# Performance work log

Hardware: AMD Instinct MI355X
Metric: run time of the kernel (lower is better)

## Reference

```python
import jax, jax.numpy as jnp
import numpy as np

# dims
B, L, HID = 4, 4096, 1024
H, D = 16, 64            # num_mem_heads, head_dim = HID // H
DM = 128                 # mem_intermediate = head_dim * mem_expansion_factor (2.0)
K = 4                    # conv_kernel
CS = 64                  # chunk_size
EPS = 1e-6


def setup_inputs() -> dict:
    key = jax.random.key(0)
    ks = jax.random.split(key, 16)
    std = 0.02
    f = lambda i, shape: jax.random.normal(ks[i], shape, jnp.float32) * std
    return {
        'hidden_states': jax.random.normal(ks[0], (B, L, HID), jnp.float32),
        'Wq': f(1, (HID, HID)), 'Wk': f(2, (HID, HID)), 'Wv': f(3, (HID, HID)),
        'conv_q_w': f(4, (HID, K)), 'conv_q_b': jnp.zeros((HID,), jnp.float32),
        'conv_k_w': f(5, (HID, K)), 'conv_k_b': jnp.zeros((HID,), jnp.float32),
        'conv_v_w': f(6, (HID, K)), 'conv_v_b': jnp.zeros((HID,), jnp.float32),
        'q_norm_w': jnp.ones((D,), jnp.float32), 'k_norm_w': jnp.ones((D,), jnp.float32),
        'mem_decay_w': f(7, (H, HID)), 'mem_decay_b': jnp.zeros((H,), jnp.float32),
        'surprise_w': f(8, (H, HID)), 'surprise_b': jnp.zeros((H,), jnp.float32),
        'lr_w': f(9, (H, HID)), 'lr_b': jnp.zeros((H,), jnp.float32),
        'W1': f(10, (H, D, DM)), 'W2': f(11, (H, DM, D)),
    }


def _silu_bwd(x):
    sig = jax.nn.sigmoid(x)
    return sig + jax.nn.silu(x) * (1.0 - sig)


def _rmsnorm(x, w):
    xf = x.astype(jnp.float32)
    var = jnp.mean(xf * xf, axis=-1, keepdims=True)
    return w * (xf * jax.lax.rsqrt(var + EPS)).astype(x.dtype)


def _causal_conv_silu(x, w, b):
    # x: [B, L, H, D] -> depthwise causal conv over time on C=H*D channels -> [B, H, L, D]
    Bs, Ls, Hh, Dd = x.shape
    xc = jnp.swapaxes(x.reshape(Bs, Ls, Hh * Dd), 1, 2)        # [B, C, L]
    xp = jnp.pad(xc, ((0, 0), (0, 0), (K - 1, 0)))             # left pad -> causal
    y = b[None, :, None]
    for k in range(K):
        y = y + w[None, :, k:k + 1] * xp[:, :, k:k + Ls]
    y = jax.nn.silu(y)
    return jnp.swapaxes(y.reshape(Bs, Hh, Dd, Ls), -2, -1)     # [B, H, L, D]


def _decayed_scan(d, v, init):
    # y_t = d_t * y_{t-1} + v_t, y_0 = init; d: [B,H,C,1], v: [B,H,C,dim], init: [B,H,1,dim]
    def comb(x, y):
        a1, b1 = x
        a2, b2 = y
        return a1 * a2, b1 * a2 + b2
    A, Bv = jax.lax.associative_scan(comb, (d, v), axis=2)
    return A * init + Bv


def _forward(hidden_states, Wq, Wk, Wv, conv_q_w, conv_q_b, conv_k_w, conv_k_b,
             conv_v_w, conv_v_b, q_norm_w, k_norm_w, mem_decay_w, mem_decay_b,
             surprise_w, surprise_b, lr_w, lr_b, W1, W2):
    x = hidden_states
    # projections -> [B, L, H, D]
    q = (x @ Wq.T).reshape(B, L, H, D)
    k = (x @ Wk.T).reshape(B, L, H, D)
    v = (x @ Wv.T).reshape(B, L, H, D)
    # depthwise causal conv + silu -> [B, H, L, D]
    q = _causal_conv_silu(q, conv_q_w, conv_q_b)
    k = _causal_conv_silu(k, conv_k_w, conv_k_b)
    v = _causal_conv_silu(v, conv_v_w, conv_v_b)
    # QK RMSNorm (per head_dim)
    q = _rmsnorm(q, q_norm_w)
    k = _rmsnorm(k, k_norm_w)
    # per-timestep gates -> [B, H, L, 1]
    mem_decay = 1.0 - jax.nn.sigmoid(x @ mem_decay_w.T + mem_decay_b)
    surprise_decay = jax.nn.sigmoid(x @ surprise_w.T + surprise_b)
    lr = jax.nn.sigmoid(x @ lr_w.T + lr_b)
    to_gate = lambda g: jnp.swapaxes(g, -2, -1)[..., None]
    mem_decay, surprise_decay, lr = to_gate(mem_decay), to_gate(surprise_decay), to_gate(lr)

    # split sequence into chunks: [N, B, H, CS, *]
    N = L // CS
    ch = lambda t: jnp.moveaxis(t.reshape(B, H, N, CS, t.shape[-1]), 2, 0)
    qs, ks_, vs = ch(q), ch(k), ch(v)
    mds, sds, lrs = ch(mem_decay), ch(surprise_decay), ch(lr)

    W1b = jnp.broadcast_to(W1[None], (B, H, D, DM))
    W2b = jnp.broadcast_to(W2[None], (B, H, DM, D))
    carry0 = (W1b, W2b,
              jnp.zeros((B, H, 1, DM), jnp.float32),   # W1_surprise
              jnp.zeros((B, H, 1, D), jnp.float32),    # W2_surprise
              jnp.zeros((B, H, 1, D), jnp.float32),    # key_momentum
              jnp.zeros((B, H, 1, DM), jnp.float32))   # X1_momentum

    def step(carry, inp):
        W1c, W2c, W1s, W2s, kmom, xmom = carry
        qc, kc, vc, md, sd, lrc = inp
        # memory MLP fwd with chunk-frozen weights
        Z1 = kc @ W1c                       # [B,H,CS,DM]
        X1 = jax.nn.silu(Z1)
        mems = X1 @ W2c                     # [B,H,CS,D]
        g_m = mems - vc
        g_Z1 = (g_m @ jnp.swapaxes(W2c, -2, -1)) * _silu_bwd(Z1)
        g_m = -lrc * g_m
        g_Z1 = -lrc * g_Z1
        # activation-space surprise/momentum scans (decayed linear recurrence)
        W1s_n = _decayed_scan(sd, g_Z1, W1s)[:, :, -1:, :]
        W2s_n = _decayed_scan(sd, g_m, W2s)[:, :, -1:, :]
        kmom_n = _decayed_scan(md, kc, kmom)[:, :, -1:, :]
        xmom_n = _decayed_scan(md, X1, xmom)[:, :, -1:, :]
        # weight update at chunk boundary: decay + outer-product of accumulated factors
        mprod = jnp.prod(md, axis=2, keepdims=True)          # [B,H,1,1]
        W1n = mprod * W1c + jnp.swapaxes(kmom_n, -2, -1) @ W1s_n
        W2n = mprod * W2c + jnp.swapaxes(xmom_n, -2, -1) @ W2s_n
        # retrieve with updated memory
        y = jax.nn.silu(qc @ W1n) @ W2n                      # [B,H,CS,D]
        return (W1n, W2n, W1s_n, W2s_n, kmom_n, xmom_n), y

    _, ys = jax.lax.scan(step, carry0, (qs, ks_, vs, mds, sds, lrs))
    mem_states = jnp.moveaxis(ys, 0, 2).reshape(B, H, L, D)
    # replicate torch: mem_states.transpose(-2,-1).reshape(B, L, H*D)
    return jnp.swapaxes(mem_states, -2, -1).reshape(B, L, H * D)


def reference(hidden_states, Wq, Wk, Wv, conv_q_w, conv_q_b, conv_k_w, conv_k_b,
              conv_v_w, conv_v_b, q_norm_w, k_norm_w, mem_decay_w, mem_decay_b,
              surprise_w, surprise_b, lr_w, lr_b, W1, W2):
    return _forward(hidden_states, Wq, Wk, Wv, conv_q_w, conv_q_b, conv_k_w, conv_k_b,
                    conv_v_w, conv_v_b, q_norm_w, k_norm_w, mem_decay_w, mem_decay_b,
                    surprise_w, surprise_b, lr_w, lr_b, W1, W2)
```

## Files before the change

kernel.cpp:

```cpp
#include <hip/hip_runtime.h>

#define B_ 4
#define L_ 4096
#define HID_ 1024
#define H_ 16
#define D_ 64
#define DM_ 128
#define CS_ 64
#define NCH_ 64
#define EPS_ 1e-6f

typedef __attribute__((ext_vector_type(8))) short bfrag_t;
typedef __attribute__((ext_vector_type(4))) float facc_t;

#define MFMA16(a,b,c) __builtin_amdgcn_mfma_f32_16x16x32_bf16(a,b,c,0,0,0)

__device__ __forceinline__ float sigf(float x){ return 1.0f/(1.0f + __expf(-x)); }

__device__ __forceinline__ unsigned f2bfu(float x){
  unsigned u = __float_as_uint(x);
  return (u + 0x7fffu + ((u>>16)&1u)) >> 16;
}
__device__ __forceinline__ float bf2f(unsigned short s){
  return __uint_as_float(((unsigned)s)<<16);
}

#define DPP_ADD_(x, ctrl) x += __int_as_float(__builtin_amdgcn_update_dpp(0, __float_as_int(x), ctrl, 0xf, 0xf, true))
__device__ __forceinline__ float wsum64(float x){
  DPP_ADD_(x, 0x111);
  DPP_ADD_(x, 0x112);
  DPP_ADD_(x, 0x114);
  DPP_ADD_(x, 0x118);
  const float a = __int_as_float(__builtin_amdgcn_readlane(__float_as_int(x), 15));
  const float b = __int_as_float(__builtin_amdgcn_readlane(__float_as_int(x), 31));
  const float c = __int_as_float(__builtin_amdgcn_readlane(__float_as_int(x), 47));
  const float d = __int_as_float(__builtin_amdgcn_readlane(__float_as_int(x), 63));
  return (a+b)+(c+d);
}

__global__ __launch_bounds__(256) void cast_kernel(
    const float* __restrict__ x,  const float* __restrict__ wq,
    const float* __restrict__ wk, const float* __restrict__ wv,
    unsigned short* __restrict__ xb,  unsigned short* __restrict__ wqb,
    unsigned short* __restrict__ wkb, unsigned short* __restrict__ wvb)
{
  const int bid = blockIdx.x;
  const float* s; unsigned short* d; int base;
  if (bid < 16384){ s = x; d = xb; base = bid*1024; }
  else {
    int r = bid - 16384; const int a = r >> 10; r &= 1023; base = r*1024;
    s = (a==0)?wq:(a==1)?wk:wv;
    d = (a==0)?wqb:(a==1)?wkb:wvb;
  }
  const int i = base + threadIdx.x*4;
  float4 v = *(const float4*)(s + i);
  unsigned lo = f2bfu(v.x) | (f2bfu(v.y)<<16);
  unsigned hi = f2bfu(v.z) | (f2bfu(v.w)<<16);
  uint2 o; o.x = lo; o.y = hi;
  *(uint2*)(d + i) = o;
}

__global__ __launch_bounds__(256, 2) void gemm_bf16_nt(
    const unsigned short* __restrict__ A, const unsigned short* __restrict__ Bw,
    unsigned short* __restrict__ C, int M, int N, int K)
{
  __shared__ __align__(16) unsigned short As[128*32];
  __shared__ __align__(16) unsigned short Bs[128*32];
  const int tid = threadIdx.x;
  const int lane = tid & 63, wave = tid >> 6;
  const int lq = lane & 15, quad = lane >> 4;
  const int m0 = blockIdx.y*128, n0 = blockIdx.x*128;
  const int row = tid >> 2, ks = (tid & 3)*8;
  const int mo = (wave & 1)*64, no = (wave >> 1)*64;

  const unsigned short* pa0 = A  + (size_t)(m0 + row)*K + ks;
  const unsigned short* pa1 = pa0 + (size_t)64*K;
  const unsigned short* pb0 = Bw + (size_t)(n0 + row)*K + ks;
  const unsigned short* pb1 = pb0 + (size_t)64*K;

  uint4 ra0 = *(const uint4*)pa0;
  uint4 ra1 = *(const uint4*)pa1;
  uint4 rb0 = *(const uint4*)pb0;
  uint4 rb1 = *(const uint4*)pb1;

  facc_t acc[4][4];
  #pragma unroll
  for (int i=0;i<4;++i)
    #pragma unroll
    for (int j=0;j<4;++j) acc[i][j] = (facc_t){0.f,0.f,0.f,0.f};

  const int kiters = K >> 5;
  for (int kt = 0; kt < kiters; ++kt){
    *(uint4*)&As[row*32 + ks]      = ra0;
    *(uint4*)&As[(row+64)*32 + ks] = ra1;
    *(uint4*)&Bs[row*32 + ks]      = rb0;
    *(uint4*)&Bs[(row+64)*32 + ks] = rb1;
    __syncthreads();
    if (kt+1 < kiters){
      const int off = (kt+1)*32;
      ra0 = *(const uint4*)(pa0 + off);
      ra1 = *(const uint4*)(pa1 + off);
      rb0 = *(const uint4*)(pb0 + off);
      rb1 = *(const uint4*)(pb1 + off);
    }
    bfrag_t af[4], bf[4];
    #pragma unroll
    for (int mt=0;mt<4;++mt) af[mt] = *(const bfrag_t*)&As[(mo+mt*16+lq)*32 + quad*8];
    #pragma unroll
    for (int nt=0;nt<4;++nt) bf[nt] = *(const bfrag_t*)&Bs[(no+nt*16+lq)*32 + quad*8];
    #pragma unroll
    for (int mt=0;mt<4;++mt)
      #pragma unroll
      for (int nt=0;nt<4;++nt)
        acc[mt][nt] = MFMA16(af[mt], bf[nt], acc[mt][nt]);
    __syncthreads();
  }

  #pragma unroll
  for (int mt=0;mt<4;++mt)
    #pragma unroll
    for (int nt=0;nt<4;++nt)
      #pragma unroll
      for (int r=0;r<4;++r){
        const int rr = m0 + mo + mt*16 + quad*4 + r;
        const int cc = n0 + no + nt*16 + lq;
        const int t = cc >> 10, hh = (cc >> 6) & 15, dd = cc & 63;
        const int b = rr >> 12, l = rr & 4095;
        C[((((size_t)t*B_ + b)*H_ + hh)*L_ + l)*64 + dd]
            = (unsigned short)f2bfu(acc[mt][nt][r]);
      }
}

__global__ __launch_bounds__(256, 2) void gates_kernel(
  const float* __restrict__ x,
  const float* __restrict__ mdw, const float* __restrict__ mdb,
  const float* __restrict__ sw,  const float* __restrict__ sb,
  const float* __restrict__ lw,  const float* __restrict__ lb,
  float* __restrict__ cmb, float* __restrict__ c1b, float* __restrict__ ppb)
{
  __shared__ float xs[64][68];
  __shared__ float wg[48][68];
  const int tid = threadIdx.x;
  const int m0 = blockIdx.x * 64;
  const int tx = tid & 15, ty = tid >> 4;
  float acc[4][3];
  #pragma unroll
  for (int r=0;r<4;++r){ acc[r][0]=0.f; acc[r][1]=0.f; acc[r][2]=0.f; }

  for (int k0 = 0; k0 < HID_; k0 += 64){
    {
      const int r = tid >> 2, kq = tid & 3;
      const float* xp = x + (size_t)(m0 + r) * HID_ + k0 + kq*16;
      #pragma unroll
      for (int u=0;u<4;++u){
        float4 v = *(const float4*)(xp + u*4);
        *(float4*)&xs[r][kq*16 + u*4] = v;
      }
    }
    #pragma unroll
    for (int u=0;u<3;++u){
      const int idx = tid + 256*u;
      const int gi = idx >> 4, q = idx & 15;
      const float* wp = (gi < 16) ? (mdw + (size_t)gi*HID_)
                      : (gi < 32) ? (sw  + (size_t)(gi-16)*HID_)
                                  : (lw  + (size_t)(gi-32)*HID_);
      float4 v = *(const float4*)(wp + k0 + q*4);
      *(float4*)&wg[gi][q*4] = v;
    }
    __syncthreads();
    for (int kk=0; kk<64; ++kk){
      float xv[4], wv[3];
      #pragma unroll
      for (int r=0;r<4;++r) xv[r] = xs[ty*4+r][kk];
      #pragma unroll
      for (int gg=0;gg<3;++gg) wv[gg] = wg[tx*3+gg][kk];
      #pragma unroll
      for (int r=0;r<4;++r)
        #pragma unroll
        for (int gg=0;gg<3;++gg) acc[r][gg] += xv[r]*wv[gg];
    }
    __syncthreads();
  }

  float (*ls)[68] = xs;
  #pragma unroll
  for (int gg=0; gg<3; ++gg){
    const int gi = tx*3 + gg;
    const int s = gi >> 4, hh = gi & 15;
    const float bias = (s==0) ? mdb[hh] : (s==1) ? sb[hh] : lb[hh];
    #pragma unroll
    for (int r=0;r<4;++r) ls[gi][ty*4+r] = acc[r][gg] + bias;
  }
  __syncthreads();

  const int lane = tid & 63, wv2 = tid >> 6;
  const int b = m0 >> 12, n = (m0 & 4095) >> 6;
  #pragma unroll
  for (int u=0;u<4;++u){
    const int hh = wv2*4 + u;
    const float md = 1.0f - sigf(ls[hh][lane]);
    const float sd = sigf(ls[16+hh][lane]);
    const float lr = sigf(ls[32+hh][lane]);
    float vm = md, vs = sd;
    #pragma unroll
    for (int off = 1; off < 64; off <<= 1){
      float om = __shfl_down(vm, off);
      float os = __shfl_down(vs, off);
      if (lane + off < 64){ vm *= om; vs *= os; }
    }
    float mex = __shfl_down(vm, 1);
    float sex = __shfl_down(vs, 1);
    if (lane == 63){ mex = 1.0f; sex = 1.0f; }
    const size_t base = ((size_t)(b*16 + hh)*NCH_ + n)*64;
    cmb[base + lane] = mex;
    c1b[base + lane] = -lr * sex;
    if (lane == 0){
      ppb[((size_t)(b*16+hh)*NCH_ + n)*2 + 0] = vm;
      ppb[((size_t)(b*16+hh)*NCH_ + n)*2 + 1] = vs;
    }
  }
}

#define HALO_T_ ((size_t)64*64*3*64)

__global__ __launch_bounds__(192) void halo_kernel(
  const unsigned short* __restrict__ qg, const unsigned short* __restrict__ kg,
  const unsigned short* __restrict__ vg, unsigned short* __restrict__ halo)
{
  const int blk = blockIdx.x;
  const int bh = blk / 63;
  const int ch = blk % 63 + 1;
  const int tid = threadIdx.x;
  const int tt = tid >> 6, lane = tid & 63;
  const long src = ((long)bh*L_ + (long)ch*64 - 3 + tt)*64 + lane;
  const long dst = (((long)bh*64 + ch)*3 + tt)*64 + lane;
  halo[dst]               = qg[src];
  halo[dst +   HALO_T_]   = kg[src];
  halo[dst + 2*HALO_T_]   = vg[src];
}

__global__ __launch_bounds__(256) void prep_kernel(
  unsigned short* __restrict__ qg, unsigned short* __restrict__ kg,
  unsigned short* __restrict__ vg,
  const unsigned short* __restrict__ halo,
  const float* __restrict__ cmg,
  const float* __restrict__ cqw, const float* __restrict__ cqb,
  const float* __restrict__ ckw, const float* __restrict__ ckb,
  const float* __restrict__ cvw, const float* __restrict__ cvb,
  const float* __restrict__ qnw, const float* __restrict__ knw,
  float* __restrict__ kredg)
{
  const int blk = blockIdx.x;
  const int bh = blk >> 6, ch = blk & 63;
  const int tid = threadIdx.x;
  const int lane = tid & 63, wave = tid >> 6;
  const int h = bh & 15;
  const int c = h*64 + lane;

  float wq4[4], wk4[4], wv4[4];
  #pragma unroll
  for (int kk=0;kk<4;++kk){ wq4[kk]=cqw[c*4+kk]; wk4[kk]=ckw[c*4+kk]; wv4[kk]=cvw[c*4+kk]; }
  const float bq = cqb[c], bk = ckb[c], bv = cvb[c];
  const float qnf = qnw[lane], knf = knw[lane];

  const long base = ((long)bh*L_ + (long)ch*64)*64 + lane;
  const int r0 = wave*16;

  float qw_[3], kw_[3], vw_[3];
  #pragma unroll
  for (int t=0;t<3;++t){
    const int row = r0 - 3 + t;
    if (row >= 0){
      qw_[t] = bf2f(qg[base + (long)row*64]);
      kw_[t] = bf2f(kg[base + (long)row*64]);
      vw_[t] = bf2f(vg[base + (long)row*64]);
    } else if (ch == 0){
      qw_[t] = 0.f; kw_[t] = 0.f; vw_[t] = 0.f;
    } else {
      const long hb = (((long)bh*64 + ch)*3 + (row + 3))*64 + lane;
      qw_[t] = bf2f(halo[hb]);
      kw_[t] = bf2f(halo[hb +   HALO_T_]);
      vw_[t] = bf2f(halo[hb + 2*HALO_T_]);
    }
  }
  __syncthreads();

  const float* cmp = cmg + ((size_t)bh*NCH_ + ch)*64;
  float kp = 0.f;
  #pragma unroll 8
  for (int i=0;i<16;++i){
    const int row = r0 + i;
    const long a = base + (long)row*64;
    const float q0v = bf2f(qg[a]);
    const float k0v = bf2f(kg[a]);
    const float v0v = bf2f(vg[a]);
    float aq = bq + wq4[0]*qw_[0] + wq4[1]*qw_[1] + wq4[2]*qw_[2] + wq4[3]*q0v;
    float ak = bk + wk4[0]*kw_[0] + wk4[1]*kw_[1] + wk4[2]*kw_[2] + wk4[3]*k0v;
    float av = bv + wv4[0]*vw_[0] + wv4[1]*vw_[1] + wv4[2]*vw_[2] + wv4[3]*v0v;
    const float yk = ak*sigf(ak), yq = aq*sigf(aq), yv = av*sigf(av);
    const float ssk = wsum64(yk*yk);
    const float ssq = wsum64(yq*yq);
    const float vk = knf * yk * rsqrtf(ssk*(1.0f/64.0f) + EPS_);
    const float vq = qnf * yq * rsqrtf(ssq*(1.0f/64.0f) + EPS_);
    const unsigned short kb16 = (unsigned short)f2bfu(vk);
    qg[a] = (unsigned short)f2bfu(vq);
    kg[a] = kb16;
    vg[a] = (unsigned short)f2bfu(yv);
    kp += cmp[row] * bf2f(kb16);
    qw_[0]=qw_[1]; qw_[1]=qw_[2]; qw_[2]=q0v;
    kw_[0]=kw_[1]; kw_[1]=kw_[2]; kw_[2]=k0v;
    vw_[0]=vw_[1]; vw_[1]=vw_[2]; vw_[2]=v0v;
  }

  __shared__ float kpart[4][64];
  kpart[wave][lane] = kp;
  __syncthreads();
  if (wave == 0)
    kredg[((size_t)bh*NCH_ + ch)*64 + lane] =
        (kpart[0][lane]+kpart[1][lane]) + (kpart[2][lane]+kpart[3][lane]);
}

#define SK 72
#define SX 136

__global__ __launch_bounds__(1024, 4) void scan_kernel(
  const unsigned short* __restrict__ qg, const unsigned short* __restrict__ kg,
  const unsigned short* __restrict__ vg,
  const float* __restrict__ cmg, const float* __restrict__ c1g,
  const float* __restrict__ ppg, const float* __restrict__ krg,
  const float* __restrict__ W1in, const float* __restrict__ W2in,
  float* __restrict__ out)
{
  const int bh = blockIdx.x;
  const int h = bh & 15;
  const int tid = threadIdx.x;
  const int lane = tid & 63, wave = tid >> 6;
  const int lq = lane & 15, quad = lane >> 4;
  const int rw = (wave & 3) * 16;
  const int cw = wave >> 2;

  __shared__ __align__(16) unsigned short sm[63488];
  unsigned short* xbs = sm + 27648;
  unsigned short* W1T = sm + 36352;
  unsigned short* W2n = sm + 45568;
  unsigned short* W2T = sm + 54784;
  __shared__ float cmA[2][64], c1A[2][64], krA[2][64], ppS[2][2];
  __shared__ float kmomS[64], xmomS[128], w1momS[128], w2momS[64];

  {
    const int j = tid >> 3, q0 = (tid & 7) * 8;
    const float* w1p = W1in + (size_t)h * D_ * DM_;
    #pragma unroll
    for (int t=0;t<8;++t)
      W1T[j*SK + q0 + t] = (unsigned short)f2bfu(w1p[(size_t)(q0+t)*DM_ + j]);
    const float* w2p = W2in + (size_t)h * DM_ * D_ + (size_t)j*D_ + q0;
    #pragma unroll
    for (int t=0;t<8;++t){
      unsigned short v = (unsigned short)f2bfu(w2p[t]);
      W2n[j*SK + q0 + t] = v;
      W2T[(q0+t)*SX + j] = v;
    }
  }
  if (tid < 64){ kmomS[tid]=0.f; w2momS[tid]=0.f; }
  if (tid < 128){ xmomS[tid]=0.f; w1momS[tid]=0.f; }

  const long cbase = (long)bh * L_ * 64;
  const int tr = tid >> 4, tc = (tid & 15) * 4;

  uint2 rq2, rk2, rv2;
  float cmr=0.f, c1r=0.f, krr=0.f, ppr=0.f;

  auto stage_load = [&](int m){
    if (m >= NCH_) return;
    const long a = cbase + ((long)m*64 + tr)*64 + tc;
    rq2 = *(const uint2*)(qg + a);
    rk2 = *(const uint2*)(kg + a);
    rv2 = *(const uint2*)(vg + a);
    if (wave == 0){
      cmr = cmg[((size_t)bh*NCH_ + m)*64 + lane];
      c1r = c1g[((size_t)bh*NCH_ + m)*64 + lane];
      krr = krg[((size_t)bh*NCH_ + m)*64 + lane];
    }
    if (tid < 2) ppr = ppg[((size_t)bh*NCH_ + m)*2 + tid];
  };

  auto stage_store = [&](int m, int s){
    if (m >= NCH_) return;
    unsigned short* kc = sm + s*4608;
    unsigned short* qc = sm + 9216 + s*4608;
    unsigned short* gm = sm + 18432 + s*4608;
    *(uint2*)&kc[tr*SK + tc] = rk2;
    *(uint2*)&qc[tr*SK + tc] = rq2;
    *(uint2*)&gm[tr*SK + tc] = rv2;
    if (wave == 0){ cmA[s][lane] = cmr; c1A[s][lane] = c1r; krA[s][lane] = krr; }
    if (tid < 2) ppS[s][tid] = ppr;
  };

  stage_load(0);
  stage_store(0, 0);
  __syncthreads();

  for (int n = 0; n < NCH_; ++n){
    const int cur = n & 1, nxt = cur ^ 1;
    const unsigned short* kcs = sm + cur*4608;
    const unsigned short* qcs = sm + 9216 + cur*4608;
    unsigned short* gms = sm + 18432 + cur*4608;

    stage_load(n+1);

    facc_t zk[2];
    {
      const bfrag_t a0 = *(const bfrag_t*)&kcs[(rw+lq)*SK + quad*8];
      const bfrag_t a1 = *(const bfrag_t*)&kcs[(rw+lq)*SK + 32 + quad*8];
      #pragma unroll
      for (int nt=0;nt<2;++nt){
        const int j = cw*32 + nt*16 + lq;
        const bfrag_t b0 = *(const bfrag_t*)&W1T[j*SK + quad*8];
        const bfrag_t b1 = *(const bfrag_t*)&W1T[j*SK + 32 + quad*8];
        facc_t z = {0.f,0.f,0.f,0.f};
        z = MFMA16(a0,b0,z); z = MFMA16(a1,b1,z);
        zk[nt] = z;
        const int r0 = rw + quad*4;
        #pragma unroll
        for (int r=0;r<4;++r)
          xbs[(r0+r)*SX + j] = (unsigned short)f2bfu(z[r]*sigf(z[r]));
      }
    }
    __syncthreads();

    {
      bfrag_t xa[4];
      #pragma unroll
      for (int kt=0;kt<4;++kt) xa[kt] = *(const bfrag_t*)&xbs[(rw+lq)*SX + kt*32 + quad*8];
      const int e = cw*16 + lq;
      facc_t z = {0.f,0.f,0.f,0.f};
      #pragma unroll
      for (int kt=0;kt<4;++kt){
        const bfrag_t bb = *(const bfrag_t*)&W2T[e*SX + kt*32 + quad*8];
        z = MFMA16(xa[kt], bb, z);
      }
      const int r0 = rw + quad*4;
      #pragma unroll
      for (int r=0;r<4;++r){
        const float g = z[r] - bf2f(gms[(r0+r)*SK + e]);
        gms[(r0+r)*SK + e] = (unsigned short)f2bfu(g);
      }
    }
    if (tid < 64) kmomS[tid] = ppS[cur][0]*kmomS[tid] + krA[cur][tid];
    {
      const int j = tid >> 3, s8 = tid & 7;
      float a0 = 0.f, a1 = 0.f;
      #pragma unroll
      for (int ii=0; ii<8; ii+=2){
        const int i0 = s8*8 + ((ii     + s8) & 7);
        const int i1 = s8*8 + ((ii + 1 + s8) & 7);
        a0 += cmA[cur][i0] * bf2f(xbs[i0*SX + j]);
        a1 += cmA[cur][i1] * bf2f(xbs[i1*SX + j]);
      }
      float xp = a0 + a1;
      xp += __shfl_xor(xp, 1);
      xp += __shfl_xor(xp, 2);
      xp += __shfl_xor(xp, 4);
      if (s8 == 0) xmomS[j] = ppS[cur][0]*xmomS[j] + xp;
    }
    stage_store(n+1, nxt);
    __syncthreads();

    {
      const bfrag_t a0 = *(const bfrag_t*)&gms[(rw+lq)*SK + quad*8];
      const bfrag_t a1 = *(const bfrag_t*)&gms[(rw+lq)*SK + 32 + quad*8];
      #pragma unroll
      for (int nt=0;nt<2;++nt){
        const int j = cw*32 + nt*16 + lq;
        const bfrag_t b0 = *(const bfrag_t*)&W2n[j*SK + quad*8];
        const bfrag_t b1 = *(const bfrag_t*)&W2n[j*SK + 32 + quad*8];
        facc_t gz = {0.f,0.f,0.f,0.f};
        gz = MFMA16(a0,b0,gz); gz = MFMA16(a1,b1,gz);
        const int r0 = rw + quad*4;
        #pragma unroll
        for (int r=0;r<4;++r){
          const float zz = zk[nt][r];
          const float sg = sigf(zz);
          xbs[(r0+r)*SX + j] = (unsigned short)f2bfu(gz[r] * (sg * (1.0f + zz*(1.0f - sg))));
        }
      }
    }
    __syncthreads();

    {
      const int j = tid >> 3, s8 = tid & 7;
      float a0 = 0.f, a1 = 0.f;
      #pragma unroll
      for (int ii=0; ii<8; ii+=2){
        const int i0 = s8*8 + ((ii     + s8) & 7);
        const int i1 = s8*8 + ((ii + 1 + s8) & 7);
        a0 += c1A[cur][i0] * bf2f(xbs[i0*SX + j]);
        a1 += c1A[cur][i1] * bf2f(xbs[i1*SX + j]);
      }
      float wp = a0 + a1;
      wp += __shfl_xor(wp, 1);
      wp += __shfl_xor(wp, 2);
      wp += __shfl_xor(wp, 4);
      if (s8 == 0) w1momS[j] = ppS[cur][1]*w1momS[j] + wp;
    }
    {
      const int e = tid >> 4, s16 = tid & 15;
      float a0 = 0.f, a1 = 0.f;
      #pragma unroll
      for (int ii=0; ii<4; ii+=2){
        const int i0 = s16*4 + ((ii     + s16) & 3);
        const int i1 = s16*4 + ((ii + 1 + s16) & 3);
        a0 += c1A[cur][i0] * bf2f(gms[i0*SK + e]);
        a1 += c1A[cur][i1] * bf2f(gms[i1*SK + e]);
      }
      float wp = a0 + a1;
      wp += __shfl_xor(wp, 1);
      wp += __shfl_xor(wp, 2);
      wp += __shfl_xor(wp, 4);
      wp += __shfl_xor(wp, 8);
      if (s16 == 0) w2momS[e] = ppS[cur][1]*w2momS[e] + wp;
    }
    __syncthreads();

    {
      const float Pmd = ppS[cur][0];
      const int j = tid >> 3, q0 = (tid & 7)*8;
      const float wm = w1momS[j], xm = xmomS[j];
      {
        const int off = j*SK + q0;
        bfrag_t wv = *(const bfrag_t*)&W1T[off];
        alignas(16) unsigned short o[8];
        #pragma unroll
        for (int s2=0;s2<8;++s2)
          o[s2] = (unsigned short)f2bfu(Pmd*bf2f((unsigned short)wv[s2]) + wm*kmomS[q0+s2]);
        *(bfrag_t*)&W1T[off] = *(const bfrag_t*)o;
      }
      {
        const int off = j*SK + q0;
        bfrag_t wv = *(const bfrag_t*)&W2n[off];
        alignas(16) unsigned short o[8];
        #pragma unroll
        for (int s2=0;s2<8;++s2)
          o[s2] = (unsigned short)f2bfu(Pmd*bf2f((unsigned short)wv[s2]) + xm*w2momS[q0+s2]);
        *(bfrag_t*)&W2n[off] = *(const bfrag_t*)o;
      }
      const int e2 = tid >> 4, js = (tid & 15)*8;
      const float w2m = w2momS[e2];
      {
        const int off = e2*SX + js;
        bfrag_t wv = *(const bfrag_t*)&W2T[off];
        alignas(16) unsigned short o[8];
        #pragma unroll
        for (int s2=0;s2<8;++s2)
          o[s2] = (unsigned short)f2bfu(Pmd*bf2f((unsigned short)wv[s2]) + xmomS[js+s2]*w2m);
        *(bfrag_t*)&W2T[off] = *(const bfrag_t*)o;
      }
    }
    __syncthreads();

    {
      const bfrag_t a0 = *(const bfrag_t*)&qcs[(rw+lq)*SK + quad*8];
      const bfrag_t a1 = *(const bfrag_t*)&qcs[(rw+lq)*SK + 32 + quad*8];
      #pragma unroll
      for (int nt=0;nt<2;++nt){
        const int j = cw*32 + nt*16 + lq;
        const bfrag_t b0 = *(const bfrag_t*)&W1T[j*SK + quad*8];
        const bfrag_t b1 = *(const bfrag_t*)&W1T[j*SK + 32 + quad*8];
        facc_t z = {0.f,0.f,0.f,0.f};
        z = MFMA16(a0,b0,z); z = MFMA16(a1,b1,z);
        const int r0 = rw + quad*4;
        #pragma unroll
        for (int r=0;r<4;++r)
          xbs[(r0+r)*SX + j] = (unsigned short)f2bfu(z[r]*sigf(z[r]));
      }
    }
    __syncthreads();

    {
      bfrag_t xa[4];
      #pragma unroll
      for (int kt=0;kt<4;++kt) xa[kt] = *(const bfrag_t*)&xbs[(rw+lq)*SX + kt*32 + quad*8];
      const int e = cw*16 + lq;
      facc_t y = {0.f,0.f,0.f,0.f};
      #pragma unroll
      for (int kt=0;kt<4;++kt){
        const bfrag_t bb = *(const bfrag_t*)&W2T[e*SX + kt*32 + quad*8];
        y = MFMA16(xa[kt], bb, y);
      }
      float4 ov; ov.x = y[0]; ov.y = y[1]; ov.z = y[2]; ov.w = y[3];
      *(float4*)&out[(size_t)bh*D_*L_ + (size_t)e*L_ + n*64 + rw + quad*4] = ov;
    }
    __syncthreads();
  }
}

extern "C" void kernel_launch(void* const* d_in, const int* in_sizes, int n_in,
                              void* d_out, int out_size, void* d_ws, size_t ws_size,
                              hipStream_t stream)
{
  const float* x   = (const float*)d_in[0];
  const float* Wq  = (const float*)d_in[1];
  const float* Wk  = (const float*)d_in[2];
  const float* Wv  = (const float*)d_in[3];
  const float* cqw = (const float*)d_in[4];
  const float* cqb = (const float*)d_in[5];
  const float* ckw = (const float*)d_in[6];
  const float* ckb = (const float*)d_in[7];
  const float* cvw = (const float*)d_in[8];
  const float* cvb = (const float*)d_in[9];
  const float* qnw = (const float*)d_in[10];
  const float* knw = (const float*)d_in[11];
  const float* mdw = (const float*)d_in[12];
  const float* mdb = (const float*)d_in[13];
  const float* sw  = (const float*)d_in[14];
  const float* sb  = (const float*)d_in[15];
  const float* lw  = (const float*)d_in[16];
  const float* lb  = (const float*)d_in[17];
  const float* W1  = (const float*)d_in[18];
  const float* W2  = (const float*)d_in[19];
  float* out = (float*)d_out;

  const size_t SZ  = (size_t)B_ * L_ * HID_;
  const size_t WSZ = (size_t)HID_ * HID_;
  unsigned short* xb  = (unsigned short*)d_ws;
  unsigned short* wqb = xb  + SZ;
  unsigned short* wkb = wqb + WSZ;
  unsigned short* wvb = wkb + WSZ;
  unsigned short* qb  = wvb + WSZ;
  unsigned short* kb  = qb  + SZ;
  unsigned short* vb  = kb  + SZ;
  float* cmb = (float*)(vb + SZ);
  float* c1b = cmb + (size_t)B_*H_*NCH_*64;
  float* ppb = c1b + (size_t)B_*H_*NCH_*64;
  float* kredg = ppb + (size_t)B_*H_*NCH_*2;
  unsigned short* halo = (unsigned short*)(kredg + (size_t)B_*H_*NCH_*64);

  cast_kernel<<<16384 + 3*1024, 256, 0, stream>>>(x, Wq, Wk, Wv, xb, wqb, wkb, wvb);
  dim3 gg(3*HID_/128, (B_*L_)/128);
  gemm_bf16_nt<<<gg, 256, 0, stream>>>(xb, wqb, qb, B_*L_, 3*HID_, HID_);
  gates_kernel<<<(B_*L_)/64, 256, 0, stream>>>(x, mdw, mdb, sw, sb, lw, lb, cmb, c1b, ppb);
  halo_kernel<<<64*63, 192, 0, stream>>>(qb, kb, vb, halo);
  prep_kernel<<<B_*H_*NCH_, 256, 0, stream>>>(qb, kb, vb, halo, cmb,
                                              cqw, cqb, ckw, ckb, cvw, cvb,
                                              qnw, knw, kredg);
  scan_kernel<<<B_*H_, 1024, 0, stream>>>(qb, kb, vb, cmb, c1b, ppb, kredg,
                                          W1, W2, out);
}
```

Before: 847.3 us.

## Fuse momentum reductions into MFMA epilogues and async-load GEMM tiles to LDS

In the scan kernel, the weighted column reductions that build the x, W1 and W2 momentum vectors now happen inside the MFMA epilogues. They use per-wave partial sums reduced with shuffles, which removes a separate reduction pass and one block-wide barrier per chunk. Float-to-bf16 packing now uses the hardware v_cvt_pk_bf16_f32 instruction instead of software rounding, and the memory update works on packed uint4 words. The projection GEMM switches to double-buffered global_load_lds direct-to-LDS loads in place of register staging. The reductions now use values before bf16 rounding and a different summation order, so results may differ slightly, and the GEMM relies on async LDS loads being visible after the barrier.

```diff
diff --git a/kernel.cpp b/kernel.cpp
--- a/kernel.cpp
+++ b/kernel.cpp
@@ -23,6 +23,20 @@
 }
 __device__ __forceinline__ float bf2f(unsigned short s){
   return __uint_as_float(((unsigned)s)<<16);
+}
+__device__ __forceinline__ unsigned cvtpk(float lo, float hi){
+  unsigned r;
+  asm("v_cvt_pk_bf16_f32 %0, %1, %2" : "=v"(r) : "v"(lo), "v"(hi));
+  return r;
+}
+__device__ __forceinline__ float bflo(unsigned u){ return __uint_as_float(u<<16); }
+__device__ __forceinline__ float bfhi(unsigned u){ return __uint_as_float(u & 0xffff0000u); }
+
+__device__ __forceinline__ void gld16(const unsigned short* g, unsigned short* l){
+  __builtin_amdgcn_global_load_lds(
+      (const __attribute__((address_space(1))) unsigned int*)(const void*)g,
+      (__attribute__((address_space(3))) unsigned int*)(void*)l,
+      16, 0, 0);
 }
 
 #define DPP_ADD_(x, ctrl) x += __int_as_float(__builtin_amdgcn_update_dpp(0, __float_as_int(x), ctrl, 0xf, 0xf, true))
@@ -64,8 +78,8 @@
     const unsigned short* __restrict__ A, const unsigned short* __restrict__ Bw,
     unsigned short* __restrict__ C, int M, int N, int K)
 {
-  __shared__ __align__(16) unsigned short As[128*32];
-  __shared__ __align__(16) unsigned short Bs[128*32];
+  __shared__ __align__(16) unsigned short As[2][4096];
+  __shared__ __align__(16) unsigned short Bs[2][4096];
   const int tid = threadIdx.x;
   const int lane = tid & 63, wave = tid >> 6;
   const int lq = lane & 15, quad = lane >> 4;
@@ -78,42 +92,41 @@
   const unsigned short* pb0 = Bw + (size_t)(n0 + row)*K + ks;
   const unsigned short* pb1 = pb0 + (size_t)64*K;
 
-  uint4 ra0 = *(const uint4*)pa0;
-  uint4 ra1 = *(const uint4*)pa1;
-  uint4 rb0 = *(const uint4*)pb0;
-  uint4 rb1 = *(const uint4*)pb1;
-
   facc_t acc[4][4];
   #pragma unroll
   for (int i=0;i<4;++i)
     #pragma unroll
     for (int j=0;j<4;++j) acc[i][j] = (facc_t){0.f,0.f,0.f,0.f};
 
+  auto stage = [&](int buf, int kt){
+    const int off = kt*32;
+    unsigned short* ab = &As[buf][wave*512];
+    unsigned short* bb = &Bs[buf][wave*512];
+    gld16(pa0 + off, ab);
+    gld16(pa1 + off, ab + 2048);
+    gld16(pb0 + off, bb);
+    gld16(pb1 + off, bb + 2048);
+  };
+
   const int kiters = K >> 5;
+  stage(0, 0);
+  __syncthreads();
+
+  int cur = 0;
   for (int kt = 0; kt < kiters; ++kt){
-    *(uint4*)&As[row*32 + ks]      = ra0;
-    *(uint4*)&As[(row+64)*32 + ks] = ra1;
-    *(uint4*)&Bs[row*32 + ks]      = rb0;
-    *(uint4*)&Bs[(row+64)*32 + ks] = rb1;
-    __syncthreads();
-    if (kt+1 < kiters){
-      const int off = (kt+1)*32;
-      ra0 = *(const uint4*)(pa0 + off);
-      ra1 = *(const uint4*)(pa1 + off);
-      rb0 = *(const uint4*)(pb0 + off);
-      rb1 = *(const uint4*)(pb1 + off);
-    }
+    if (kt+1 < kiters) stage(cur^1, kt+1);
     bfrag_t af[4], bf[4];
     #pragma unroll
-    for (int mt=0;mt<4;++mt) af[mt] = *(const bfrag_t*)&As[(mo+mt*16+lq)*32 + quad*8];
-    #pragma unroll
-    for (int nt=0;nt<4;++nt) bf[nt] = *(const bfrag_t*)&Bs[(no+nt*16+lq)*32 + quad*8];
+    for (int mt=0;mt<4;++mt) af[mt] = *(const bfrag_t*)&As[cur][(mo+mt*16+lq)*32 + quad*8];
+    #pragma unroll
+    for (int nt=0;nt<4;++nt) bf[nt] = *(const bfrag_t*)&Bs[cur][(no+nt*16+lq)*32 + quad*8];
     #pragma unroll
     for (int mt=0;mt<4;++mt)
       #pragma unroll
       for (int nt=0;nt<4;++nt)
         acc[mt][nt] = MFMA16(af[mt], bf[nt], acc[mt][nt]);
     __syncthreads();
+    cur ^= 1;
   }
 
   #pragma unroll
@@ -336,7 +349,8 @@
   const int tid = threadIdx.x;
   const int lane = tid & 63, wave = tid >> 6;
   const int lq = lane & 15, quad = lane >> 4;
-  const int rw = (wave & 3) * 16;
+  const int wg = wave & 3;
+  const int rw = wg * 16;
   const int cw = wave >> 2;
 
   __shared__ __align__(16) unsigned short sm[63488];
@@ -346,6 +360,7 @@
   unsigned short* W2T = sm + 54784;
   __shared__ float cmA[2][64], c1A[2][64], krA[2][64], ppS[2][2];
   __shared__ float kmomS[64], xmomS[128], w1momS[128], w2momS[64];
+  __shared__ float xpart[4][128], w1part[4][128], w2part[4][64];
 
   {
     const int j = tid >> 3, q0 = (tid & 7) * 8;
@@ -405,6 +420,7 @@
     const unsigned short* kcs = sm + cur*4608;
     const unsigned short* qcs = sm + 9216 + cur*4608;
     unsigned short* gms = sm + 18432 + cur*4608;
+    const int r0 = rw + quad*4;
 
     stage_load(n+1);
 
@@ -412,6 +428,7 @@
     {
       const bfrag_t a0 = *(const bfrag_t*)&kcs[(rw+lq)*SK + quad*8];
       const bfrag_t a1 = *(const bfrag_t*)&kcs[(rw+lq)*SK + 32 + quad*8];
+      const float4 cmv = *(const float4*)&cmA[cur][r0];
       #pragma unroll
       for (int nt=0;nt<2;++nt){
         const int j = cw*32 + nt*16 + lq;
@@ -420,10 +437,17 @@
         facc_t z = {0.f,0.f,0.f,0.f};
         z = MFMA16(a0,b0,z); z = MFMA16(a1,b1,z);
         zk[nt] = z;
-        const int r0 = rw + quad*4;
-        #pragma unroll
-        for (int r=0;r<4;++r)
-          xbs[(r0+r)*SX + j] = (unsigned short)f2bfu(z[r]*sigf(z[r]));
+        const float x0 = z[0]*sigf(z[0]), x1 = z[1]*sigf(z[1]);
+        const float x2 = z[2]*sigf(z[2]), x3 = z[3]*sigf(z[3]);
+        const unsigned p01 = cvtpk(x0,x1), p23 = cvtpk(x2,x3);
+        xbs[(r0+0)*SX + j] = (unsigned short)p01;
+        xbs[(r0+1)*SX + j] = (unsigned short)(p01>>16);
+        xbs[(r0+2)*SX + j] = (unsigned short)p23;
+        xbs[(r0+3)*SX + j] = (unsigned short)(p23>>16);
+        float xp = cmv.x*x0 + cmv.y*x1 + cmv.z*x2 + cmv.w*x3;
+        xp += __shfl_xor(xp, 16);
+        xp += __shfl_xor(xp, 32);
+        if (quad == 0) xpart[wg][j] = xp;
       }
     }
     __syncthreads();
@@ -439,36 +463,32 @@
         const bfrag_t bb = *(const bfrag_t*)&W2T[e*SX + kt*32 + quad*8];
         z = MFMA16(xa[kt], bb, z);
       }
-      const int r0 = rw + quad*4;
-      #pragma unroll
-      for (int r=0;r<4;++r){
-        const float g = z[r] - bf2f(gms[(r0+r)*SK + e]);
-        gms[(r0+r)*SK + e] = (unsigned short)f2bfu(g);
-      }
+      const float g0 = z[0] - bf2f(gms[(r0+0)*SK + e]);
+      const float g1 = z[1] - bf2f(gms[(r0+1)*SK + e]);
+      const float g2 = z[2] - bf2f(gms[(r0+2)*SK + e]);
+      const float g3 = z[3] - bf2f(gms[(r0+3)*SK + e]);
+      const unsigned p01 = cvtpk(g0,g1), p23 = cvtpk(g2,g3);
+      gms[(r0+0)*SK + e] = (unsigned short)p01;
+      gms[(r0+1)*SK + e] = (unsigned short)(p01>>16);
+      gms[(r0+2)*SK + e] = (unsigned short)p23;
+      gms[(r0+3)*SK + e] = (unsigned short)(p23>>16);
+      const float4 c1v = *(const float4*)&c1A[cur][r0];
+      float wp = c1v.x*g0 + c1v.y*g1 + c1v.z*g2 + c1v.w*g3;
+      wp += __shfl_xor(wp, 16);
+      wp += __shfl_xor(wp, 32);
+      if (quad == 0) w2part[wg][e] = wp;
     }
     if (tid < 64) kmomS[tid] = ppS[cur][0]*kmomS[tid] + krA[cur][tid];
-    {
-      const int j = tid >> 3, s8 = tid & 7;
-      float a0 = 0.f, a1 = 0.f;
-      #pragma unroll
-      for (int ii=0; ii<8; ii+=2){
-        const int i0 = s8*8 + ((ii     + s8) & 7);
-        const int i1 = s8*8 + ((ii + 1 + s8) & 7);
-        a0 += cmA[cur][i0] * bf2f(xbs[i0*SX + j]);
-        a1 += cmA[cur][i1] * bf2f(xbs[i1*SX + j]);
-      }
-      float xp = a0 + a1;
-      xp += __shfl_xor(xp, 1);
-      xp += __shfl_xor(xp, 2);
-      xp += __shfl_xor(xp, 4);
-      if (s8 == 0) xmomS[j] = ppS[cur][0]*xmomS[j] + xp;
-    }
+    if (tid < 128)
+      xmomS[tid] = ppS[cur][0]*xmomS[tid]
+                 + ((xpart[0][tid]+xpart[1][tid])+(xpart[2][tid]+xpart[3][tid]));
     stage_store(n+1, nxt);
     __syncthreads();
 
     {
       const bfrag_t a0 = *(const bfrag_t*)&gms[(rw+lq)*SK + quad*8];
       const bfrag_t a1 = *(const bfrag_t*)&gms[(rw+lq)*SK + 32 + quad*8];
+      const float4 c1v = *(const float4*)&c1A[cur][r0];
       #pragma unroll
       for (int nt=0;nt<2;++nt){
         const int j = cw*32 + nt*16 + lq;
@@ -476,84 +496,73 @@
         const bfrag_t b1 = *(const bfrag_t*)&W2n[j*SK + 32 + quad*8];
         facc_t gz = {0.f,0.f,0.f,0.f};
         gz = MFMA16(a0,b0,gz); gz = MFMA16(a1,b1,gz);
-        const int r0 = rw + quad*4;
+        float d[4];
         #pragma unroll
         for (int r=0;r<4;++r){
           const float zz = zk[nt][r];
           const float sg = sigf(zz);
-          xbs[(r0+r)*SX + j] = (unsigned short)f2bfu(gz[r] * (sg * (1.0f + zz*(1.0f - sg))));
+          d[r] = gz[r] * (sg * (1.0f + zz*(1.0f - sg)));
         }
-      }
-    }
+        const unsigned p01 = cvtpk(d[0],d[1]), p23 = cvtpk(d[2],d[3]);
+        xbs[(r0+0)*SX + j] = (unsigned short)p01;
+        xbs[(r0+1)*SX + j] = (unsigned short)(p01>>16);
+        xbs[(r0+2)*SX + j] = (unsigned short)p23;
+        xbs[(r0+3)*SX + j] = (unsigned short)(p23>>16);
+        float wp = c1v.x*d[0] + c1v.y*d[1] + c1v.z*d[2] + c1v.w*d[3];
+        wp += __shfl_xor(wp, 16);
+        wp += __shfl_xor(wp, 32);
+        if (quad == 0) w1part[wg][j] = wp;
+      }
+    }
+    if (tid < 64)
+      w2momS[tid] = ppS[cur][1]*w2momS[tid]
+                  + ((w2part[0][tid]+w2part[1][tid])+(w2part[2][tid]+w2part[3][tid]));
     __syncthreads();
 
     {
-      const int j = tid >> 3, s8 = tid & 7;
-      float a0 = 0.f, a1 = 0.f;
-      #pragma unroll
-      for (int ii=0; ii<8; ii+=2){
-        const int i0 = s8*8 + ((ii     + s8) & 7);
-        const int i1 = s8*8 + ((ii + 1 + s8) & 7);
-        a0 += c1A[cur][i0] * bf2f(xbs[i0*SX + j]);
-        a1 += c1A[cur][i1] * bf2f(xbs[i1*SX + j]);
-      }
-      float wp = a0 + a1;
-      wp += __shfl_xor(wp, 1);
-      wp += __shfl_xor(wp, 2);
-      wp += __shfl_xor(wp, 4);
-      if (s8 == 0) w1momS[j] = ppS[cur][1]*w1momS[j] + wp;
-    }
-    {
-      const int e = tid >> 4, s16 = tid & 15;
-      float a0 = 0.f, a1 = 0.f;
-      #pragma unroll
-      for (int ii=0; ii<4; ii+=2){
-        const int i0 = s16*4 + ((ii     + s16) & 3);
-        const int i1 = s16*4 + ((ii + 1 + s16) & 3);
-        a0 += c1A[cur][i0] * bf2f(gms[i0*SK + e]);
-        a1 += c1A[cur][i1] * bf2f(gms[i1*SK + e]);
-      }
-      float wp = a0 + a1;
-      wp += __shfl_xor(wp, 1);
-      wp += __shfl_xor(wp, 2);
-      wp += __shfl_xor(wp, 4);
-      wp += __shfl_xor(wp, 8);
-      if (s16 == 0) w2momS[e] = ppS[cur][1]*w2momS[e] + wp;
-    }
-    __syncthreads();
-
-    {
-      const float Pmd = ppS[cur][0];
+      const float Pmd = ppS[cur][0], Psd = ppS[cur][1];
       const int j = tid >> 3, q0 = (tid & 7)*8;
-      const float wm = w1momS[j], xm = xmomS[j];
+      const float w1m = Psd*w1momS[j]
+          + ((w1part[0][j]+w1part[1][j])+(w1part[2][j]+w1part[3][j]));
+      if ((tid & 7) == 0) w1momS[j] = w1m;
+      const float xm = xmomS[j];
+      const float4 km0 = *(const float4*)&kmomS[q0];
+      const float4 km1 = *(const float4*)&kmomS[q0+4];
       {
         const int off = j*SK + q0;
-        bfrag_t wv = *(const bfrag_t*)&W1T[off];
-        alignas(16) unsigned short o[8];
-        #pragma unroll
-        for (int s2=0;s2<8;++s2)
-          o[s2] = (unsigned short)f2bfu(Pmd*bf2f((unsigned short)wv[s2]) + wm*kmomS[q0+s2]);
-        *(bfrag_t*)&W1T[off] = *(const bfrag_t*)o;
-      }
+        const uint4 w = *(const uint4*)&W1T[off];
+        uint4 o;
+        o.x = cvtpk(Pmd*bflo(w.x) + w1m*km0.x, Pmd*bfhi(w.x) + w1m*km0.y);
+        o.y = cvtpk(Pmd*bflo(w.y) + w1m*km0.z, Pmd*bfhi(w.y) + w1m*km0.w);
+        o.z = cvtpk(Pmd*bflo(w.z) + w1m*km1.x, Pmd*bfhi(w.z) + w1m*km1.y);
+        o.w = cvtpk(Pmd*bflo(w.w) + w1m*km1.z, Pmd*bfhi(w.w) + w1m*km1.w);
+        *(uint4*)&W1T[off] = o;
+      }
+      const float4 wm0 = *(const float4*)&w2momS[q0];
+      const float4 wm1 = *(const float4*)&w2momS[q0+4];
       {
         const int off = j*SK + q0;
-        bfrag_t wv = *(const bfrag_t*)&W2n[off];
-        alignas(16) unsigned short o[8];
-        #pragma unroll
-        for (int s2=0;s2<8;++s2)
-          o[s2] = (unsigned short)f2bfu(Pmd*bf2f((unsigned short)wv[s2]) + xm*w2momS[q0+s2]);
-        *(bfrag_t*)&W2n[off] = *(const bfrag_t*)o;
+        const uint4 w = *(const uint4*)&W2n[off];
+        uint4 o;
+        o.x = cvtpk(Pmd*bflo(w.x) + xm*wm0.x, Pmd*bfhi(w.x) + xm*wm0.y);
+        o.y = cvtpk(Pmd*bflo(w.y) + xm*wm0.z, Pmd*bfhi(w.y) + xm*wm0.w);
+        o.z = cvtpk(Pmd*bflo(w.z) + xm*wm1.x, Pmd*bfhi(w.z) + xm*wm1.y);
+        o.w = cvtpk(Pmd*bflo(w.w) + xm*wm1.z, Pmd*bfhi(w.w) + xm*wm1.w);
+        *(uint4*)&W2n[off] = o;
       }
       const int e2 = tid >> 4, js = (tid & 15)*8;
       const float w2m = w2momS[e2];
+      const float4 xm0 = *(const float4*)&xmomS[js];
+      const float4 xm1 = *(const float4*)&xmomS[js+4];
       {
         const int off = e2*SX + js;
-        bfrag_t wv = *(const bfrag_t*)&W2T[off];
-        alignas(16) unsigned short o[8];
-        #pragma unroll
-        for (int s2=0;s2<8;++s2)
-          o[s2] = (unsigned short)f2bfu(Pmd*bf2f((unsigned short)wv[s2]) + xmomS[js+s2]*w2m);
-        *(bfrag_t*)&W2T[off] = *(const bfrag_t*)o;
+        const uint4 w = *(const uint4*)&W2T[off];
+        uint4 o;
+        o.x = cvtpk(Pmd*bflo(w.x) + xm0.x*w2m, Pmd*bfhi(w.x) + xm0.y*w2m);
+        o.y = cvtpk(Pmd*bflo(w.y) + xm0.z*w2m, Pmd*bfhi(w.y) + xm0.w*w2m);
+        o.z = cvtpk(Pmd*bflo(w.z) + xm1.x*w2m, Pmd*bfhi(w.z) + xm1.y*w2m);
+        o.w = cvtpk(Pmd*bflo(w.w) + xm1.z*w2m, Pmd*bfhi(w.w) + xm1.w*w2m);
+        *(uint4*)&W2T[off] = o;
       }
     }
     __syncthreads();
@@ -568,10 +577,13 @@
         const bfrag_t b1 = *(const bfrag_t*)&W1T[j*SK + 32 + quad*8];
         facc_t z = {0.f,0.f,0.f,0.f};
         z = MFMA16(a0,b0,z); z = MFMA16(a1,b1,z);
-        const int r0 = rw + quad*4;
-        #pragma unroll
-        for (int r=0;r<4;++r)
-          xbs[(r0+r)*SX + j] = (unsigned short)f2bfu(z[r]*sigf(z[r]));
+        const float x0 = z[0]*sigf(z[0]), x1 = z[1]*sigf(z[1]);
+        const float x2 = z[2]*sigf(z[2]), x3 = z[3]*sigf(z[3]);
+        const unsigned p01 = cvtpk(x0,x1), p23 = cvtpk(x2,x3);
+        xbs[(r0+0)*SX + j] = (unsigned short)p01;
+        xbs[(r0+1)*SX + j] = (unsigned short)(p01>>16);
+        xbs[(r0+2)*SX + j] = (unsigned short)p23;
+        xbs[(r0+3)*SX + j] = (unsigned short)(p23>>16);
       }
     }
     __syncthreads();
```

Result: faster. 772.6 us (-8.8%).
